# Optimization experiments

Hardware: AMD Instinct MI355X
Metric: run time of the kernel (lower is better)

## Reference

```python
import jax, jax.numpy as jnp
import numpy as np

B, S, H, NH, DEPTH = 8, 1024, 1024, 16, 24
MLP = int(H * 4.0)
EPS = 1e-6


def _ln(z):
    # flax LayerNorm(use_bias=False, use_scale=False, dtype=bf16): stats in fp32, output bf16
    m = jnp.mean(z, axis=-1, keepdims=True)
    v = jnp.mean(jnp.square(z - m), axis=-1, keepdims=True)
    return ((z - m) * jax.lax.rsqrt(v + EPS)).astype(jnp.bfloat16)


def _modulate(x, shift, scale):
    return x * scale[:, None] + shift[:, None]


def _rms(x):
    return jnp.sqrt(jnp.mean(jnp.square(x)))


def setup_inputs() -> dict:
    key = jax.random.key(0)
    ks = jax.random.split(key, 7)
    init = lambda k, shape, std: (jax.random.normal(k, shape, dtype=jnp.float32) * std)
    return {
        "x": jax.random.normal(ks[0], (B, S, H), dtype=jnp.float32),
        "c": jax.random.normal(ks[1], (B, H), dtype=jnp.float32),
        "w_cond": init(ks[2], (H, 6 * H), 0.02),
        "w_qkv": init(ks[3], (H, 3 * H), 0.02),
        "w_attn_out": init(ks[4], (H, H), 0.02 / np.sqrt(2 * DEPTH)),
        "w_mlp1": init(ks[5], (H, MLP), 0.02),
        "w_mlp2": init(ks[6], (MLP, H), 0.02 / np.sqrt(2 * DEPTH)),
    }


def reference(x, c, w_cond, w_qkv, w_attn_out, w_mlp1, w_mlp2):
    dh = H // NH
    # adaLN conditioning
    cm = jax.nn.silu(c) @ w_cond  # [B, 6H]
    shift_msa, scale_msa, gate_msa, shift_mlp, scale_mlp, gate_mlp = jnp.split(cm, 6, axis=-1)

    # --- attention ---
    x_mod = _modulate(_ln(x), shift_msa, scale_msa)  # fp32 after promote
    kqv = x_mod @ w_qkv
    k, q, v = jnp.split(kqv, 3, axis=-1)
    k = k.reshape(B, S, NH, dh)
    q = q.reshape(B, S, NH, dh) / jnp.sqrt(jnp.float32(dh))
    v = v.reshape(B, S, NH, dh)
    w = jnp.einsum('bqhc,bkhc->bhqk', q, k).astype(jnp.float32)
    w = jax.nn.softmax(w, axis=-1)
    info_max_attn_weight = jnp.mean(jnp.max(w, axis=-1))
    y = jnp.einsum('bhqk,bkhc->bqhc', w, v).reshape(x.shape)
    x_attn = gate_msa[:, None] * (y @ w_attn_out)
    info_attn_norm_ratio = _rms(x_attn) / _rms(x)
    x = x + x_attn

    # --- MLP ---
    x_mod2 = _modulate(_ln(x), shift_mlp, scale_mlp)
    x_mlp = x_mod2 @ w_mlp1
    frac_pos = jnp.mean(x_mlp > 0, axis=(0, 1))
    info_relu_diff = jnp.mean(jnp.abs(frac_pos - 0.5))
    info_relu_zero = jnp.mean(frac_pos == 0)
    info_relu_positive = jnp.mean(frac_pos == 1)
    info_relu_norm = _rms(x_mlp)
    x_mlp = jax.nn.gelu(x_mlp)
    x_mlp = gate_mlp[:, None] * (x_mlp @ w_mlp2)
    info_mlp_norm_ratio = _rms(x_mlp) / _rms(x)
    x = x + x_mlp
    return (x, (info_relu_diff, info_relu_zero, info_relu_positive,
                info_max_attn_weight, info_attn_norm_ratio, info_mlp_norm_ratio,
                info_relu_norm))
```

## Files before the change

kernel.cpp:

```cpp
#include <hip/hip_runtime.h>

typedef unsigned short u16;
typedef __bf16 bf16x8 __attribute__((ext_vector_type(8)));
typedef unsigned short u16x8 __attribute__((ext_vector_type(8)));
typedef float f32x4 __attribute__((ext_vector_type(4)));

union V8 { u16x8 u; bf16x8 b; };

__device__ __forceinline__ u16 f2bf(float f) {
    unsigned u = __float_as_uint(f);
    u += 0x7fffu + ((u >> 16) & 1u);
    return (u16)(u >> 16);
}
__device__ __forceinline__ float bf2f(u16 h) {
    return __uint_as_float(((unsigned)h) << 16);
}

__device__ __forceinline__ void gld16(const void* g, void* l) {
    __builtin_amdgcn_global_load_lds(
        (const __attribute__((address_space(1))) void*)g,
        (__attribute__((address_space(3))) void*)l, 16, 0, 0);
}

__device__ __forceinline__ float block_sum256(float v, float* red) {
#pragma unroll
    for (int mk = 1; mk < 64; mk <<= 1) v += __shfl_xor(v, mk);
    __syncthreads();
    if ((threadIdx.x & 63) == 0) red[threadIdx.x >> 6] = v;
    __syncthreads();
    return red[0] + red[1] + red[2] + red[3];
}

__global__ __launch_bounds__(256)
void cond_kernel(const float* __restrict__ c, const float* __restrict__ w,
                 float* __restrict__ cm) {
    __shared__ float sc[1024];
    const int b = blockIdx.y;
    for (int i = threadIdx.x; i < 1024; i += 256) {
        float v = c[b * 1024 + i];
        sc[i] = v / (1.f + expf(-v));
    }
    __syncthreads();
    const int col = blockIdx.x * 256 + threadIdx.x;
    float acc = 0.f;
    for (int i = 0; i < 1024; ++i) acc += sc[i] * w[(size_t)i * 6144 + col];
    cm[b * 6144 + col] = acc;
}

__global__ __launch_bounds__(256)
void ln_mod_kernel(const float* __restrict__ x, const float* __restrict__ cm,
                   int shift0, int scale0, u16* __restrict__ out) {
    __shared__ float red[8];
    const int row = blockIdx.x, tid = threadIdx.x;
    const int b = row >> 10;
    const float4 v = *(const float4*)(x + (size_t)row * 1024 + tid * 4);
    float s = v.x + v.y + v.z + v.w;
#pragma unroll
    for (int mk = 1; mk < 64; mk <<= 1) s += __shfl_xor(s, mk);
    if ((tid & 63) == 0) red[tid >> 6] = s;
    __syncthreads();
    const float mean = (red[0] + red[1] + red[2] + red[3]) * (1.f / 1024.f);
    const float d0 = v.x - mean, d1 = v.y - mean, d2 = v.z - mean, d3 = v.w - mean;
    float ss = d0 * d0 + d1 * d1 + d2 * d2 + d3 * d3;
#pragma unroll
    for (int mk = 1; mk < 64; mk <<= 1) ss += __shfl_xor(ss, mk);
    if ((tid & 63) == 0) red[4 + (tid >> 6)] = ss;
    __syncthreads();
    const float var = (red[4] + red[5] + red[6] + red[7]) * (1.f / 1024.f);
    const float rs = rsqrtf(var + 1e-6f);
    const float* cmb = cm + b * 6144;
    const int c0 = tid * 4;
    ushort4 ov;
    ov.x = f2bf(bf2f(f2bf(d0 * rs)) * cmb[scale0 + c0 + 0] + cmb[shift0 + c0 + 0]);
    ov.y = f2bf(bf2f(f2bf(d1 * rs)) * cmb[scale0 + c0 + 1] + cmb[shift0 + c0 + 1]);
    ov.z = f2bf(bf2f(f2bf(d2 * rs)) * cmb[scale0 + c0 + 2] + cmb[shift0 + c0 + 2]);
    ov.w = f2bf(bf2f(f2bf(d3 * rs)) * cmb[scale0 + c0 + 3] + cmb[shift0 + c0 + 3]);
    *(ushort4*)(out + (size_t)row * 1024 + c0) = ov;
}

__global__ __launch_bounds__(256)
void transpose_cast(const float* __restrict__ in, u16* __restrict__ out,
                    int R, int C) {
    __shared__ float t[32][33];
    const int tx = threadIdx.x, ty = threadIdx.y;
    const int c0 = blockIdx.x * 32, r0 = blockIdx.y * 32;
#pragma unroll
    for (int i = 0; i < 4; ++i)
        t[ty + i * 8][tx] = in[(size_t)(r0 + ty + i * 8) * C + c0 + tx];
    __syncthreads();
#pragma unroll
    for (int i = 0; i < 4; ++i)
        out[(size_t)(c0 + ty + i * 8) * R + r0 + tx] = f2bf(t[tx][ty + i * 8]);
}

__global__ __launch_bounds__(256)
void vtrans_kernel(const u16* __restrict__ kqv, u16* __restrict__ vT) {
    __shared__ u16 t[32][33];
    const int tx = threadIdx.x, ty = threadIdx.y;
    const int s0 = blockIdx.x * 32, d0 = blockIdx.y * 32;
    const int bh = blockIdx.z, b = bh >> 4, h = bh & 15;
#pragma unroll
    for (int i = 0; i < 4; ++i) {
        int s = s0 + ty + i * 8;
        t[ty + i * 8][tx] = kqv[(size_t)(b * 1024 + s) * 3072 + 2048 + h * 64 + d0 + tx];
    }
    __syncthreads();
#pragma unroll
    for (int i = 0; i < 4; ++i) {
        int d = d0 + ty + i * 8;
        vT[((size_t)bh * 64 + d) * 1024 + s0 + tx] = t[tx][ty + i * 8];
    }
}

template <int EPI>
__global__ __launch_bounds__(256)
void gemm_epi(const u16* __restrict__ A, const u16* __restrict__ BT,
              int M, int N, int K,
              u16* __restrict__ outb, float* __restrict__ outf,
              const float* __restrict__ resid, const float* __restrict__ gatec,
              float* __restrict__ stats, int* __restrict__ counts) {
    __shared__ u16 As[128 * 32];
    __shared__ u16 Bs[128 * 32];
    __shared__ float red[4];
    __shared__ int ccnt[128];

    const int tid = threadIdx.x;
    const int lane = tid & 63;
    const int wave = tid >> 6;
    const int wm = wave & 1, wn = wave >> 1;
    const int quad = lane >> 4, l15 = lane & 15;
    const int tm = blockIdx.x * 128, tn = blockIdx.y * 128;

    const int srow = tid >> 2;
    const int scol = (((tid & 3) ^ ((srow >> 1) & 3))) * 8;
    const int rsw = (l15 >> 1) & 3;

    f32x4 acc[4][4];
#pragma unroll
    for (int i = 0; i < 4; ++i)
#pragma unroll
        for (int j = 0; j < 4; ++j) acc[i][j] = (f32x4){0.f, 0.f, 0.f, 0.f};

    for (int k0 = 0; k0 < K; k0 += 32) {
        __syncthreads();
#pragma unroll
        for (int p = 0; p < 2; ++p) {
            const int r = p * 64 + srow;
            gld16(A + (size_t)(tm + r) * K + k0 + scol, As + p * 2048 + wave * 512);
            gld16(BT + (size_t)(tn + r) * K + k0 + scol, Bs + p * 2048 + wave * 512);
        }
        __syncthreads();
        V8 af[4], bfr[4];
#pragma unroll
        for (int i = 0; i < 4; ++i)
            af[i].u = *(const u16x8*)(As + (wm * 64 + i * 16 + l15) * 32 + ((quad ^ rsw) * 8));
#pragma unroll
        for (int j = 0; j < 4; ++j)
            bfr[j].u = *(const u16x8*)(Bs + (wn * 64 + j * 16 + l15) * 32 + ((quad ^ rsw) * 8));
#pragma unroll
        for (int i = 0; i < 4; ++i)
#pragma unroll
            for (int j = 0; j < 4; ++j)
                acc[i][j] = __builtin_amdgcn_mfma_f32_16x16x32_bf16(
                    af[i].b, bfr[j].b, acc[i][j], 0, 0, 0);
    }

    if (EPI == 2) {
        for (int i = tid; i < 128; i += 256) ccnt[i] = 0;
    }
    __syncthreads();

    float s0 = 0.f, s1 = 0.f, s2 = 0.f;
    int cj[4] = {0, 0, 0, 0};
#pragma unroll
    for (int i = 0; i < 4; ++i) {
#pragma unroll
        for (int j = 0; j < 4; ++j) {
#pragma unroll
            for (int r = 0; r < 4; ++r) {
                const int row = tm + wm * 64 + i * 16 + quad * 4 + r;
                const int col = tn + wn * 64 + j * 16 + l15;
                const float v = acc[i][j][r];
                const size_t idx = (size_t)row * N + col;
                if (EPI == 0) {
                    outb[idx] = f2bf(v);
                } else if (EPI == 1) {
                    const int bb = row >> 10;
                    const float g = gatec[bb * 6144 + col];
                    const float xa = g * v;
                    const float xv = resid[idx];
                    const float o = xv + xa;
                    outf[idx] = o;
                    s0 += xa * xa; s1 += xv * xv; s2 += o * o;
                } else if (EPI == 2) {
                    cj[j] += (v > 0.f) ? 1 : 0;
                    s0 += v * v;
                    const float a = fminf(0.7978845608028654f * (v + 0.044715f * v * v * v), 40.f);
                    const float e = __expf(2.f * a);
                    outb[idx] = f2bf(v * e / (e + 1.f));
                } else {
                    const int bb = row >> 10;
                    const float g = gatec[bb * 6144 + col];
                    const float xm = g * v;
                    const float o = resid[idx] + xm;
                    outf[idx] = o;
                    s0 += xm * xm;
                }
            }
        }
    }

    if (EPI == 1) {
        float t = block_sum256(s0, red); if (tid == 0) atomicAdd(&stats[0], t);
        t = block_sum256(s1, red);       if (tid == 0) atomicAdd(&stats[1], t);
        t = block_sum256(s2, red);       if (tid == 0) atomicAdd(&stats[2], t);
    } else if (EPI == 2) {
#pragma unroll
        for (int j = 0; j < 4; ++j) {
            int c = cj[j];
            c += __shfl_xor(c, 16);
            c += __shfl_xor(c, 32);
            if (quad == 0) atomicAdd(&ccnt[wn * 64 + j * 16 + l15], c);
        }
        __syncthreads();
        for (int i = tid; i < 128; i += 256) atomicAdd(&counts[tn + i], ccnt[i]);
        float t = block_sum256(s0, red); if (tid == 0) atomicAdd(&stats[3], t);
    } else if (EPI == 3) {
        float t = block_sum256(s0, red); if (tid == 0) atomicAdd(&stats[4], t);
    }
}

__global__ __launch_bounds__(256, 2)
void attn_kernel(const u16* __restrict__ kqv, const u16* __restrict__ vT,
                 u16* __restrict__ y, float* __restrict__ stats) {
    __shared__ __align__(16) char smem[49152];
    u16* Ks = (u16*)smem;
    u16* Vs = (u16*)(smem + 16384);
    u16* P  = (u16*)(smem + 32768);
    float* obuf = (float*)smem;
    float* mlb  = (float*)(smem + 32768);
    float* lbuf = (float*)(smem + 32768 + 2048);

    const int tid = threadIdx.x, lane = tid & 63, w = tid >> 6;
    const int quad = lane >> 4, l15 = lane & 15;
    const int bh = blockIdx.y, b = bh >> 4, h = bh & 15;
    const int qbase = blockIdx.x * 64;
    const int fq = (l15 >> 1) & 3;

    V8 qf[4][2];
#pragma unroll
    for (int qt = 0; qt < 4; ++qt) {
        const size_t rq = ((size_t)(b * 1024 + qbase + qt * 16 + l15)) * 3072
                        + 1024 + h * 64 + quad * 8;
        qf[qt][0].u = *(const u16x8*)(kqv + rq);
        qf[qt][1].u = *(const u16x8*)(kqv + rq + 32);
    }

    float m[4], l[4];
    f32x4 o[4][4];
#pragma unroll
    for (int qt = 0; qt < 4; ++qt) { m[qt] = -__builtin_inff(); l[qt] = 0.f; }
#pragma unroll
    for (int dt = 0; dt < 4; ++dt)
#pragma unroll
        for (int qt = 0; qt < 4; ++qt) o[dt][qt] = (f32x4){0.f, 0.f, 0.f, 0.f};

    u16* wp = P + w * 2048;
    const size_t kbase = (size_t)(b * 1024) * 3072 + h * 64;
    const size_t vbase = (size_t)bh * 65536;

    for (int k0 = 0; k0 < 1024; k0 += 128) {
        __syncthreads();
#pragma unroll
        for (int i = 0; i < 4; ++i) {
            const int c = i * 256 + tid;
            {
                const int row = c >> 3, col8 = (c & 7) ^ (row & 7);
                gld16(kqv + kbase + (size_t)(k0 + row) * 3072 + col8 * 8,
                      Ks + (i * 256 + w * 64) * 8);
            }
            {
                const int d = c >> 4, col8 = (c & 15) ^ (d & 15);
                gld16(vT + vbase + (size_t)d * 1024 + k0 + col8 * 8,
                      Vs + (i * 256 + w * 64) * 8);
            }
        }
        __syncthreads();

        f32x4 s[2][4];
#pragma unroll
        for (int kt = 0; kt < 2; ++kt) {
            const int krow = w * 32 + kt * 16 + l15;
            V8 ak0, ak1;
            ak0.u = *(const u16x8*)(Ks + krow * 64 + ((quad ^ (l15 & 7)) * 8));
            ak1.u = *(const u16x8*)(Ks + krow * 64 + (((quad + 4) ^ (l15 & 7)) * 8));
#pragma unroll
            for (int qt = 0; qt < 4; ++qt) {
                s[kt][qt] = __builtin_amdgcn_mfma_f32_16x16x32_bf16(
                    ak0.b, qf[qt][0].b, (f32x4){0.f, 0.f, 0.f, 0.f}, 0, 0, 0);
                s[kt][qt] = __builtin_amdgcn_mfma_f32_16x16x32_bf16(
                    ak1.b, qf[qt][1].b, s[kt][qt], 0, 0, 0);
            }
        }

#pragma unroll
        for (int qt = 0; qt < 4; ++qt) {
            float mx = s[0][qt][0];
            mx = fmaxf(mx, s[0][qt][1]); mx = fmaxf(mx, s[0][qt][2]);
            mx = fmaxf(mx, s[0][qt][3]); mx = fmaxf(mx, s[1][qt][0]);
            mx = fmaxf(mx, s[1][qt][1]); mx = fmaxf(mx, s[1][qt][2]);
            mx = fmaxf(mx, s[1][qt][3]);
            mx *= 0.125f;
            mx = fmaxf(mx, __shfl_xor(mx, 16));
            mx = fmaxf(mx, __shfl_xor(mx, 32));
            const float mn = fmaxf(m[qt], mx);
            const float alpha = __expf(m[qt] - mn);
            float ps = 0.f;
            u16 pr[2][4];
#pragma unroll
            for (int kt = 0; kt < 2; ++kt)
#pragma unroll
                for (int r = 0; r < 4; ++r) {
                    const float p = __expf(s[kt][qt][r] * 0.125f - mn);
                    ps += p;
                    pr[kt][r] = f2bf(p);
                }
            ps += __shfl_xor(ps, 16);
            ps += __shfl_xor(ps, 32);
            l[qt] = l[qt] * alpha + ps;
            m[qt] = mn;
#pragma unroll
            for (int dt = 0; dt < 4; ++dt) o[dt][qt] *= alpha;
            const int qrow = qt * 16 + l15;
#pragma unroll
            for (int kt = 0; kt < 2; ++kt) {
                const int c0 = (kt * 2 + (quad >> 1)) ^ fq;
                u16* pdst = wp + qrow * 32 + c0 * 8 + (quad & 1) * 4;
                *(unsigned*)(pdst)     = (unsigned)pr[kt][0] | ((unsigned)pr[kt][1] << 16);
                *(unsigned*)(pdst + 2) = (unsigned)pr[kt][2] | ((unsigned)pr[kt][3] << 16);
            }
        }

        V8 pb[4];
#pragma unroll
        for (int qt = 0; qt < 4; ++qt)
            pb[qt].u = *(const u16x8*)(wp + (qt * 16 + l15) * 32 + ((quad ^ fq) * 8));
#pragma unroll
        for (int dt = 0; dt < 4; ++dt) {
            V8 av;
            av.u = *(const u16x8*)(Vs + (dt * 16 + l15) * 128 + (((w * 4 + quad) ^ l15) * 8));
#pragma unroll
            for (int qt = 0; qt < 4; ++qt)
                o[dt][qt] = __builtin_amdgcn_mfma_f32_16x16x32_bf16(
                    av.b, pb[qt].b, o[dt][qt], 0, 0, 0);
        }
    }

    __syncthreads();
    if (quad == 0) {
#pragma unroll
        for (int qt = 0; qt < 4; ++qt) {
            mlb[(w * 4 + qt) * 16 + l15] = m[qt];
            mlb[256 + (w * 4 + qt) * 16 + l15] = l[qt];
        }
    }
    __syncthreads();
    float scale[4];
#pragma unroll
    for (int qt = 0; qt < 4; ++qt) {
        float M = -__builtin_inff();
#pragma unroll
        for (int ww = 0; ww < 4; ++ww) M = fmaxf(M, mlb[(ww * 4 + qt) * 16 + l15]);
        float L = 0.f;
#pragma unroll
        for (int ww = 0; ww < 4; ++ww)
            L += mlb[256 + (ww * 4 + qt) * 16 + l15] *
                 __expf(mlb[(ww * 4 + qt) * 16 + l15] - M);
        scale[qt] = __expf(m[qt] - M);
        if (w == 0 && quad == 0) lbuf[qt * 16 + l15] = 1.f / L;
    }
    for (int ww = 0; ww < 4; ++ww) {
        if (ww == w) {
#pragma unroll
            for (int qt = 0; qt < 4; ++qt) {
                float* dst = obuf + (qt * 16 + l15) * 72 + quad * 4;
#pragma unroll
                for (int dt = 0; dt < 4; ++dt) {
                    f32x4 v = o[dt][qt] * scale[qt];
                    if (ww != 0) v += *(f32x4*)(dst + dt * 16);
                    *(f32x4*)(dst + dt * 16) = v;
                }
            }
        }
        __syncthreads();
    }
    if (w == 0) {
        float sv = lbuf[lane];
#pragma unroll
        for (int mk = 1; mk < 64; mk <<= 1) sv += __shfl_xor(sv, mk);
        if (lane == 0) atomicAdd(&stats[5], sv);
    }
    {
        const int q = tid >> 2, dseg = (tid & 3) * 16;
        const float il = lbuf[q];
        const float* src = obuf + q * 72 + dseg;
        __align__(16) u16 tmp[16];
#pragma unroll
        for (int j = 0; j < 16; ++j) tmp[j] = f2bf(src[j] * il);
        u16* ydst = y + ((size_t)(b * 1024 + qbase + q)) * 1024 + h * 64 + dseg;
        *(uint4*)(ydst) = *(uint4*)(tmp);
        *(uint4*)(ydst + 8) = *(uint4*)(tmp + 8);
    }
}

__global__ __launch_bounds__(256)
void finalize_kernel(const int* __restrict__ counts, const float* __restrict__ stats,
                     float* __restrict__ out7) {
    __shared__ float red[4];
    float d = 0.f, z = 0.f, pp = 0.f;
    for (int i = threadIdx.x; i < 4096; i += 256) {
        const int c = counts[i];
        const float frac = (float)c * (1.f / 8192.f);
        d += fabsf(frac - 0.5f);
        z += (c == 0) ? 1.f : 0.f;
        pp += (c == 8192) ? 1.f : 0.f;
    }
    d = block_sum256(d, red);
    z = block_sum256(z, red);
    pp = block_sum256(pp, red);
    if (threadIdx.x == 0) {
        out7[0] = d * (1.f / 4096.f);
        out7[1] = z * (1.f / 4096.f);
        out7[2] = pp * (1.f / 4096.f);
        out7[3] = stats[5] * (1.f / 131072.f);
        out7[4] = sqrtf(stats[0] / stats[1]);
        out7[5] = sqrtf(stats[4] / stats[2]);
        out7[6] = sqrtf(stats[3] / (8192.f * 4096.f));
    }
}

extern "C" void kernel_launch(void* const* d_in, const int* in_sizes, int n_in,
                              void* d_out, int out_size, void* d_ws, size_t ws_size,
                              hipStream_t stream) {
    const float* x      = (const float*)d_in[0];
    const float* c      = (const float*)d_in[1];
    const float* w_cond = (const float*)d_in[2];
    const float* w_qkv  = (const float*)d_in[3];
    const float* w_attn = (const float*)d_in[4];
    const float* w_mlp1 = (const float*)d_in[5];
    const float* w_mlp2 = (const float*)d_in[6];
    float* out = (float*)d_out;

    char* base = (char*)d_ws;
    size_t off = 0;
    auto alloc = [&](size_t n) { void* r = base + off; off += (n + 255) & ~(size_t)255; return r; };
    float* stats   = (float*)alloc(64);
    int*   counts  = (int*)alloc(4096 * 4);
    float* cm      = (float*)alloc((size_t)8 * 6144 * 4);
    u16*   x_mod   = (u16*)alloc((size_t)8192 * 1024 * 2);
    u16*   kqv     = (u16*)alloc((size_t)8192 * 3072 * 2);
    u16*   vT      = (u16*)alloc((size_t)128 * 64 * 1024 * 2);
    u16*   y       = (u16*)alloc((size_t)8192 * 1024 * 2);
    float* x1      = (float*)alloc((size_t)8192 * 1024 * 4);
    u16*   wt_qkv  = (u16*)alloc((size_t)3072 * 1024 * 2);
    u16*   wt_attn = (u16*)alloc((size_t)1024 * 1024 * 2);
    u16*   wt_mlp1 = (u16*)alloc((size_t)4096 * 1024 * 2);
    u16*   wt_mlp2 = (u16*)alloc((size_t)1024 * 4096 * 2);
    u16*   h_act   = kqv;
    u16*   x_mod2  = x_mod;
    (void)vT; (void)ws_size; (void)n_in; (void)in_sizes; (void)out_size;

    hipMemsetAsync(d_ws, 0, 256 + 4096 * 4, stream);

    dim3 tb(32, 8);
    transpose_cast<<<dim3(3072 / 32, 1024 / 32), tb, 0, stream>>>(w_qkv,  wt_qkv,  1024, 3072);
    transpose_cast<<<dim3(1024 / 32, 1024 / 32), tb, 0, stream>>>(w_attn, wt_attn, 1024, 1024);
    transpose_cast<<<dim3(4096 / 32, 1024 / 32), tb, 0, stream>>>(w_mlp1, wt_mlp1, 1024, 4096);
    transpose_cast<<<dim3(1024 / 32, 4096 / 32), tb, 0, stream>>>(w_mlp2, wt_mlp2, 4096, 1024);

    cond_kernel<<<dim3(24, 8), 256, 0, stream>>>(c, w_cond, cm);

    ln_mod_kernel<<<8192, 256, 0, stream>>>(x, cm, 0, 1024, x_mod);

    gemm_epi<0><<<dim3(8192 / 128, 3072 / 128), 256, 0, stream>>>(
        x_mod, wt_qkv, 8192, 3072, 1024, kqv, nullptr, nullptr, nullptr, stats, nullptr);

    vtrans_kernel<<<dim3(32, 2, 128), tb, 0, stream>>>(kqv, vT);

    attn_kernel<<<dim3(16, 128), 256, 0, stream>>>(kqv, vT, y, stats);

    gemm_epi<1><<<dim3(8192 / 128, 1024 / 128), 256, 0, stream>>>(
        y, wt_attn, 8192, 1024, 1024, nullptr, x1, x, cm + 2 * 1024, stats, nullptr);

    ln_mod_kernel<<<8192, 256, 0, stream>>>(x1, cm, 3 * 1024, 4 * 1024, x_mod2);

    gemm_epi<2><<<dim3(8192 / 128, 4096 / 128), 256, 0, stream>>>(
        x_mod2, wt_mlp1, 8192, 4096, 1024, h_act, nullptr, nullptr, nullptr, stats, counts);

    gemm_epi<3><<<dim3(8192 / 128, 1024 / 128), 256, 0, stream>>>(
        h_act, wt_mlp2, 8192, 1024, 4096, nullptr, out, x1, cm + 5 * 1024, stats, nullptr);

    finalize_kernel<<<1, 256, 0, stream>>>(counts, stats, out + (size_t)8192 * 1024);
}
```

Measured before the change: 628.0 us.

## Batch cond kernel over all rows, hoist GEMM pointers and gate loads, faster GELU

The conditioning kernel now computes all 8 batch rows in one block per column strip, so each w_cond element is read once instead of eight times. The price is only 24 blocks and 32KB of shared memory per block. In the GEMM, the global load addresses are precomputed and advanced incrementally, and the per-column gate values are loaded once into registers instead of once per element. GELU uses a reciprocal intrinsic instead of a division, which trades a little accuracy for fewer instructions.

```diff
diff --git a/kernel.cpp b/kernel.cpp
--- a/kernel.cpp
+++ b/kernel.cpp
@@ -16,6 +16,13 @@
     return __uint_as_float(((unsigned)h) << 16);
 }
 
+__device__ __forceinline__ float gelu_fast(float v) {
+    const float p = v * fmaf(v * v, 0.044715f, 1.0f);
+    const float t = fminf(1.5957691216057308f * p, 80.f);
+    const float e = __expf(t);
+    return v * e * __builtin_amdgcn_rcpf(e + 1.f);
+}
+
 __device__ __forceinline__ void gld16(const void* g, void* l) {
     __builtin_amdgcn_global_load_lds(
         (const __attribute__((address_space(1))) void*)g,
@@ -34,17 +41,23 @@
 __global__ __launch_bounds__(256)
 void cond_kernel(const float* __restrict__ c, const float* __restrict__ w,
                  float* __restrict__ cm) {
-    __shared__ float sc[1024];
-    const int b = blockIdx.y;
-    for (int i = threadIdx.x; i < 1024; i += 256) {
-        float v = c[b * 1024 + i];
+    __shared__ float sc[8 * 1024];
+    for (int i = threadIdx.x; i < 8192; i += 256) {
+        float v = c[i];
         sc[i] = v / (1.f + expf(-v));
     }
     __syncthreads();
     const int col = blockIdx.x * 256 + threadIdx.x;
-    float acc = 0.f;
-    for (int i = 0; i < 1024; ++i) acc += sc[i] * w[(size_t)i * 6144 + col];
-    cm[b * 6144 + col] = acc;
+    float acc[8];
+#pragma unroll
+    for (int b = 0; b < 8; ++b) acc[b] = 0.f;
+    for (int i = 0; i < 1024; ++i) {
+        const float wv = w[(size_t)i * 6144 + col];
+#pragma unroll
+        for (int b = 0; b < 8; ++b) acc[b] = fmaf(sc[b * 1024 + i], wv, acc[b]);
+    }
+#pragma unroll
+    for (int b = 0; b < 8; ++b) cm[b * 6144 + col] = acc[b];
 }
 
 __global__ __launch_bounds__(256)
@@ -135,6 +148,10 @@
     const int scol = (((tid & 3) ^ ((srow >> 1) & 3))) * 8;
     const int rsw = (l15 >> 1) & 3;
 
+    const u16* pa = A + (size_t)(tm + srow) * K + scol;
+    const u16* pb = BT + (size_t)(tn + srow) * K + scol;
+    const size_t rstep = (size_t)64 * K;
+
     f32x4 acc[4][4];
 #pragma unroll
     for (int i = 0; i < 4; ++i)
@@ -143,12 +160,11 @@
 
     for (int k0 = 0; k0 < K; k0 += 32) {
         __syncthreads();
-#pragma unroll
-        for (int p = 0; p < 2; ++p) {
-            const int r = p * 64 + srow;
-            gld16(A + (size_t)(tm + r) * K + k0 + scol, As + p * 2048 + wave * 512);
-            gld16(BT + (size_t)(tn + r) * K + k0 + scol, Bs + p * 2048 + wave * 512);
-        }
+        gld16(pa, As + wave * 512);
+        gld16(pa + rstep, As + 2048 + wave * 512);
+        gld16(pb, Bs + wave * 512);
+        gld16(pb + rstep, Bs + 2048 + wave * 512);
+        pa += 32; pb += 32;
         __syncthreads();
         V8 af[4], bfr[4];
 #pragma unroll
@@ -169,6 +185,14 @@
         for (int i = tid; i < 128; i += 256) ccnt[i] = 0;
     }
     __syncthreads();
+
+    const int bb = tm >> 10;
+    float gj[4];
+    if (EPI == 1 || EPI == 3) {
+#pragma unroll
+        for (int j = 0; j < 4; ++j)
+            gj[j] = gatec[bb * 6144 + tn + wn * 64 + j * 16 + l15];
+    }
 
     float s0 = 0.f, s1 = 0.f, s2 = 0.f;
     int cj[4] = {0, 0, 0, 0};
@@ -185,9 +209,7 @@
                 if (EPI == 0) {
                     outb[idx] = f2bf(v);
                 } else if (EPI == 1) {
-                    const int bb = row >> 10;
-                    const float g = gatec[bb * 6144 + col];
-                    const float xa = g * v;
+                    const float xa = gj[j] * v;
                     const float xv = resid[idx];
                     const float o = xv + xa;
                     outf[idx] = o;
@@ -195,13 +217,9 @@
                 } else if (EPI == 2) {
                     cj[j] += (v > 0.f) ? 1 : 0;
                     s0 += v * v;
-                    const float a = fminf(0.7978845608028654f * (v + 0.044715f * v * v * v), 40.f);
-                    const float e = __expf(2.f * a);
-                    outb[idx] = f2bf(v * e / (e + 1.f));
+                    outb[idx] = f2bf(gelu_fast(v));
                 } else {
-                    const int bb = row >> 10;
-                    const float g = gatec[bb * 6144 + col];
-                    const float xm = g * v;
+                    const float xm = gj[j] * v;
                     const float o = resid[idx] + xm;
                     outf[idx] = o;
                     s0 += xm * xm;
@@ -478,7 +496,7 @@
     transpose_cast<<<dim3(4096 / 32, 1024 / 32), tb, 0, stream>>>(w_mlp1, wt_mlp1, 1024, 4096);
     transpose_cast<<<dim3(1024 / 32, 4096 / 32), tb, 0, stream>>>(w_mlp2, wt_mlp2, 4096, 1024);
 
-    cond_kernel<<<dim3(24, 8), 256, 0, stream>>>(c, w_cond, cm);
+    cond_kernel<<<24, 256, 0, stream>>>(c, w_cond, cm);
 
     ln_mod_kernel<<<8192, 256, 0, stream>>>(x, cm, 0, 1024, x_mod);
 
```

New measurement: 741.8 us. 18.1% more time.
